# Kernel optimization log

Measured on AMD Instinct MI355X. Metric: run time of the kernel, lower is better.

Reference implementation:

```python
import jax, jax.numpy as jnp
import numpy as np
import math
from jax import lax

N = 5          # kernel_size (hard-coded PHT assumes 5x5)
K = N // 2     # 2
EPS = 1e-6
THETA = 0.7

def _pht_kernel_np():
    # H_i = cos(2*pi*2*r^2 + 0*theta) on the 5x5 grid, times calibrated spectral weights, plus eps
    coords = np.arange(N, dtype=np.float32) - K
    gv, gu = np.meshgrid(coords, coords, indexing='ij')  # torch.meshgrid default is 'ij'
    r2 = (gu ** 2 + gv ** 2) / (K * K + EPS)
    H = np.cos(2.0 * math.pi * 2.0 * r2).astype(np.float32)
    target = np.zeros((N, N), np.float32)
    target[K, K] = -4.0
    target[K - 1, K] = 1.0
    target[K + 1, K] = 1.0
    target[K, K - 1] = 1.0
    target[K, K + 1] = 1.0
    sw = np.where(target != 0, target / H, 0.0).astype(np.float32)
    return (H * sw + EPS).astype(np.float32)  # (5,5)

def _rotation_maps_np():
    # Replicates rotate_kernel exactly: float32 cos/sin, int() truncation, later (h,w) overwrite.
    angles = np.linspace(0, 2 * np.pi, 8, endpoint=False)
    SH = np.zeros((8, N, N), np.int32)
    SW = np.zeros((8, N, N), np.int32)
    M = np.zeros((8, N, N), np.float32)
    for ai, a in enumerate(angles):
        c = float(np.cos(np.float32(a)))
        s = float(np.sin(np.float32(a)))
        for h in range(N):
            for w in range(N):
                rh = int(h * c + w * (-s))
                rw = int(h * s + w * c)
                if 0 <= rh < N and 0 <= rw < N:
                    SH[ai, rh, rw] = h
                    SW[ai, rh, rw] = w
                    M[ai, rh, rw] = 1.0
    return SH, SW, M

_PHT = jnp.asarray(_pht_kernel_np())                     # (5,5)
_sh, _sw, _m = _rotation_maps_np()
_SH = jnp.asarray(_sh)
_SW = jnp.asarray(_sw)
_MASK = jnp.asarray(_m)

def setup_inputs() -> dict:
    key = jax.random.key(0)
    k1, k2 = jax.random.split(key)
    x = jax.random.normal(k1, (32, 64, 128, 128), dtype=jnp.float32)
    weight = jax.random.normal(k2, (64, 64, 5, 5), dtype=jnp.float32) * 0.05
    alpha = jnp.ones((1,), dtype=jnp.float32)
    return {"x": x, "weight": weight, "alpha": alpha}

def reference(x, weight, alpha):
    # Branch 1: PHT-modulated weight, averaged over 8 SO(2) rotations.
    # pht_kernel is (C_in,1,5,5) with identical values per channel -> broadcast (5,5).
    w_eff = weight * alpha[0] * _PHT[None, None]          # (Co,Ci,5,5)
    # rotated[o,i,a,rh,rw] = w_eff[o,i,SH[a,rh,rw],SW[a,rh,rw]] * MASK
    rotated = w_eff[:, :, _SH, _SW] * _MASK               # (Co,Ci,8,5,5)
    # conv is linear in weight: mean of 8 convs == conv with mean kernel
    mean_k = rotated.mean(axis=2)                         # (Co,Ci,5,5)
    out = lax.conv_general_dilated(
        x, mean_k, window_strides=(1, 1), padding=[(2, 2), (2, 2)],
        dimension_numbers=("NCHW", "OIHW", "NCHW"))
    # Branch 2: 1x1 kernel_diff; rotation of a 1x1 kernel is identity, mean of 8 == single conv.
    kd = weight.sum(axis=(2, 3))                          # (Co,Ci)
    out_diff = jnp.einsum("oi,bihw->bohw", kd, x)
    return out - THETA * out_diff
```

## Files before the change

### kernel.cpp

```cpp
#include <hip/hip_runtime.h>
#include <stdint.h>

typedef __attribute__((ext_vector_type(8))) __bf16 bf16x8;
typedef __attribute__((ext_vector_type(16))) float f32x16;
typedef __attribute__((ext_vector_type(4))) unsigned int u32x4;
typedef __attribute__((ext_vector_type(4))) float f32x4;
typedef __attribute__((ext_vector_type(2))) float f32x2;
typedef unsigned int u32;
typedef unsigned short u16;

#define THETA 0.7f

__host__ __device__ constexpr float pht_val(int q) {
  return (q == 12) ? (-4.0f + 1e-6f)
       : (q == 7 || q == 11 || q == 13 || q == 17) ? (1.0f + 1e-6f)
       : 1e-6f;
}

__device__ __forceinline__ u16 f2bf(float v) {
  u32 u = __builtin_bit_cast(u32, v);
  return (u16)((u + 0x7fffu + ((u >> 16) & 1u)) >> 16);
}

__global__ __launch_bounds__(256) void k_prep(const float* __restrict__ wgt,
                                              const float* __restrict__ alpha,
                                              u16* __restrict__ apack) {
  int t = blockIdx.x * 256 + threadIdx.x;
  int o = t >> 6, ci = t & 63;
  const float* wp = wgt + ((size_t)(o * 64 + ci)) * 25;
  float wv[25], sumw = 0.f;
#pragma unroll
  for (int p = 0; p < 25; ++p) { wv[p] = wp[p]; sumw += wv[p]; }
  float keff[25];
#pragma unroll
  for (int p = 0; p < 25; ++p) keff[p] = pht_val(p) * wv[p];
  constexpr int TP[33] = {0,1,2,3,4,6,7,9,12,13,  0,1,2,3,4,  0, 0, 0,
                          0,5,10,15,20,  0,5,6,10,11,12,15,17,20,21};
  constexpr int TQ[33] = {5,6,12,17,23,10,16,22,20,21,  0,5,10,15,20,  5, 0, 5,
                          0,6,7,8,9,  5,6,2,12,8,4,17,9,23,14};
#pragma unroll
  for (int e = 0; e < 33; ++e) keff[TP[e]] += pht_val(TQ[e]) * wv[TQ[e]];

  float al = alpha[0];
  int kc = ci >> 4, oh = o >> 5;
  int lane = ((ci >> 3) & 1) * 32 + (o & 31);
#pragma unroll
  for (int p = 0; p < 25; ++p) {
    float v = al * (keff[p] * 0.125f);
    if (p == 12) v -= THETA * sumw;
    size_t idx = ((((size_t)p * 4 + kc) * 2 + oh) * 64 + lane) * 8 + (ci & 7);
    apack[idx] = f2bf(v);
  }
}

#define GSTR 1168
#define RSTR 2336
#define BUFSZ 18688

#define MM(A, B, C) __builtin_amdgcn_mfma_f32_32x32x16_bf16((A), __builtin_bit_cast(bf16x8, (B)), (C), 0, 0, 0)

#define PK2(A_, B_) ({ u32 r_;                                              \
    asm("v_cvt_pk_bf16_f32 %0, %1, %2" : "=v"(r_) : "v"(A_), "v"(B_));      \
    r_; })

#define LDBR(S, DX, KC) do {                                                \
    const char* pb_ = tile + (((KC) & 1) * BUFSZ) + cb0 + (DX) * 16;        \
    br##S##0 = *(const u32x4*)(pb_ + 0 * RSTR);                             \
    br##S##1 = *(const u32x4*)(pb_ + 1 * RSTR);                             \
    br##S##2 = *(const u32x4*)(pb_ + 2 * RSTR);                             \
    br##S##3 = *(const u32x4*)(pb_ + 3 * RSTR);                             \
    br##S##4 = *(const u32x4*)(pb_ + 4 * RSTR);                             \
    br##S##5 = *(const u32x4*)(pb_ + 5 * RSTR);                             \
    br##S##6 = *(const u32x4*)(pb_ + 6 * RSTR);                             \
    br##S##7 = *(const u32x4*)(pb_ + 7 * RSTR);                             \
  } while (0)

#define LDAF(S, DX, KC) do {                                                \
    af##S##0 = apb[(size_t)((0 * 5 + (DX)) * 512 + (KC) * 128)];            \
    af##S##1 = apb[(size_t)((1 * 5 + (DX)) * 512 + (KC) * 128)];            \
    af##S##2 = apb[(size_t)((2 * 5 + (DX)) * 512 + (KC) * 128)];            \
    af##S##3 = apb[(size_t)((3 * 5 + (DX)) * 512 + (KC) * 128)];            \
    af##S##4 = apb[(size_t)((4 * 5 + (DX)) * 512 + (KC) * 128)];            \
  } while (0)

#define BURST(S) do {                                                       \
    bf16x8 A_;                                                              \
    A_ = __builtin_bit_cast(bf16x8, af##S##0);                              \
    a0 = MM(A_, br##S##0, a0); a1 = MM(A_, br##S##1, a1);                   \
    a2 = MM(A_, br##S##2, a2); a3 = MM(A_, br##S##3, a3);                   \
    A_ = __builtin_bit_cast(bf16x8, af##S##1);                              \
    a0 = MM(A_, br##S##1, a0); a1 = MM(A_, br##S##2, a1);                   \
    a2 = MM(A_, br##S##3, a2); a3 = MM(A_, br##S##4, a3);                   \
    A_ = __builtin_bit_cast(bf16x8, af##S##2);                              \
    a0 = MM(A_, br##S##2, a0); a1 = MM(A_, br##S##3, a1);                   \
    a2 = MM(A_, br##S##4, a2); a3 = MM(A_, br##S##5, a3);                   \
    A_ = __builtin_bit_cast(bf16x8, af##S##3);                              \
    a0 = MM(A_, br##S##3, a0); a1 = MM(A_, br##S##4, a1);                   \
    a2 = MM(A_, br##S##5, a2); a3 = MM(A_, br##S##6, a3);                   \
    A_ = __builtin_bit_cast(bf16x8, af##S##4);                              \
    a0 = MM(A_, br##S##4, a0); a1 = MM(A_, br##S##5, a1);                   \
    a2 = MM(A_, br##S##6, a2); a3 = MM(A_, br##S##7, a3);                   \
  } while (0)

#define SGB __builtin_amdgcn_sched_group_barrier
#define SCHED_FULL() do {                                                   \
    SGB(0x020, 5, 0);                                                       \
    SGB(0x100, 2, 0); SGB(0x008, 5, 0);                                     \
    SGB(0x100, 2, 0); SGB(0x008, 5, 0);                                     \
    SGB(0x100, 2, 0); SGB(0x008, 5, 0);                                     \
    SGB(0x100, 2, 0); SGB(0x008, 5, 0);                                     \
  } while (0)

#define ITER(CUR, NXT, DXN, KCN) do {                                       \
    LDBR(NXT, DXN, KCN); LDAF(NXT, DXN, KCN); BURST(CUR); SCHED_FULL();     \
  } while (0)

#define TBAR() do {                                                         \
    asm volatile("s_waitcnt lgkmcnt(0)" ::: "memory");                      \
    __builtin_amdgcn_sched_barrier(0);                                      \
    __builtin_amdgcn_s_barrier();                                           \
    __builtin_amdgcn_sched_barrier(0);                                      \
  } while (0)

#define SLOADP(P) do {                                                      \
    if (rowok) {                                                            \
      const float* pm_ = xrow + (size_t)(16 * (P) + 8 * gp) * 16384 + pxm;  \
      sm0 = *(const f32x4*)(pm_);              sm1 = *(const f32x4*)(pm_ + 16384);      \
      sm2 = *(const f32x4*)(pm_ + 2 * 16384);  sm3 = *(const f32x4*)(pm_ + 3 * 16384);  \
      sm4 = *(const f32x4*)(pm_ + 4 * 16384);  sm5 = *(const f32x4*)(pm_ + 5 * 16384);  \
      sm6 = *(const f32x4*)(pm_ + 6 * 16384);  sm7 = *(const f32x4*)(pm_ + 7 * 16384);  \
    } else {                                                                \
      sm0 = 0; sm1 = 0; sm2 = 0; sm3 = 0; sm4 = 0; sm5 = 0; sm6 = 0; sm7 = 0; \
    }                                                                       \
    if (hdut) {                                                             \
      if (hok) {                                                            \
        const float* ph_ = xn + (size_t)hsy * 128                           \
                           + (size_t)(16 * (P) + 8 * hgp) * 16384 + hpx;    \
        sh0 = *(const f32x2*)(ph_);              sh1 = *(const f32x2*)(ph_ + 16384);     \
        sh2 = *(const f32x2*)(ph_ + 2 * 16384);  sh3 = *(const f32x2*)(ph_ + 3 * 16384); \
        sh4 = *(const f32x2*)(ph_ + 4 * 16384);  sh5 = *(const f32x2*)(ph_ + 5 * 16384); \
        sh6 = *(const f32x2*)(ph_ + 6 * 16384);  sh7 = *(const f32x2*)(ph_ + 7 * 16384); \
      } else {                                                              \
        sh0 = 0; sh1 = 0; sh2 = 0; sh3 = 0; sh4 = 0; sh5 = 0; sh6 = 0; sh7 = 0; \
      }                                                                     \
    }                                                                       \
  } while (0)

#define SWRITEP(P) do {                                                     \
    char* wb_ = tile + (((P) & 1) * BUFSZ) + rr * RSTR + gp * GSTR;         \
    u32x4 w_;                                                               \
    w_[0] = PK2(sm0.x, sm1.x); w_[1] = PK2(sm2.x, sm3.x);                   \
    w_[2] = PK2(sm4.x, sm5.x); w_[3] = PK2(sm6.x, sm7.x);                   \
    *(u32x4*)(wb_ + (cbm + 0) * 16) = w_;                                   \
    w_[0] = PK2(sm0.y, sm1.y); w_[1] = PK2(sm2.y, sm3.y);                   \
    w_[2] = PK2(sm4.y, sm5.y); w_[3] = PK2(sm6.y, sm7.y);                   \
    *(u32x4*)(wb_ + (cbm + 1) * 16) = w_;                                   \
    w_[0] = PK2(sm0.z, sm1.z); w_[1] = PK2(sm2.z, sm3.z);                   \
    w_[2] = PK2(sm4.z, sm5.z); w_[3] = PK2(sm6.z, sm7.z);                   \
    *(u32x4*)(wb_ + (cbm + 2) * 16) = w_;                                   \
    w_[0] = PK2(sm0.w, sm1.w); w_[1] = PK2(sm2.w, sm3.w);                   \
    w_[2] = PK2(sm4.w, sm5.w); w_[3] = PK2(sm6.w, sm7.w);                   \
    *(u32x4*)(wb_ + (cbm + 3) * 16) = w_;                                   \
    if (hdut) {                                                             \
      char* hb_ = tile + (((P) & 1) * BUFSZ) + hrr * RSTR + hgp * GSTR;     \
      u32x4 u_;                                                             \
      u_[0] = PK2(sh0.x, sh1.x); u_[1] = PK2(sh2.x, sh3.x);                 \
      u_[2] = PK2(sh4.x, sh5.x); u_[3] = PK2(sh6.x, sh7.x);                 \
      *(u32x4*)(hb_ + (hc + 0) * 16) = u_;                                  \
      u_[0] = PK2(sh0.y, sh1.y); u_[1] = PK2(sh2.y, sh3.y);                 \
      u_[2] = PK2(sh4.y, sh5.y); u_[3] = PK2(sh6.y, sh7.y);                 \
      *(u32x4*)(hb_ + (hc + 1) * 16) = u_;                                  \
    }                                                                       \
  } while (0)

#define CPHASE(SP, CP) do {                                                 \
    SLOADP(SP);                                                             \
    LDBR(A, 0, CP); LDAF(A, 0, CP);                                         \
    ITER(A, B, 1, CP);                                                      \
    ITER(B, A, 2, CP);                                                      \
    SWRITEP(SP);                                                            \
    ITER(A, B, 3, CP);                                                      \
    ITER(B, A, 4, CP);                                                      \
    BURST(A);                                                               \
    TBAR();                                                                 \
  } while (0)

__global__ __launch_bounds__(256, 2) void k_conv(const float* __restrict__ x,
                                                 const u32x4* __restrict__ apv,
                                                 float* __restrict__ out) {
  __shared__ char tile[2 * BUFSZ];
  int bid = blockIdx.x;
  int lg = (bid & 7) * 256 + (bid >> 3);
  int ph = lg & 1, yt = (lg >> 1) & 31, n = lg >> 6;
  int y0 = yt * 4, px0 = ph * 64;
  int tid = threadIdx.x;
  int l = tid & 63;

  const float* xn = x + (size_t)n * (64 * 16384);
  int rr = tid >> 5, qq = (tid >> 1) & 15, gp = tid & 1;
  int sy = y0 + rr - 2;
  bool rowok = (unsigned)sy < 128u;
  const float* xrow = xn + (size_t)(rowok ? sy : 0) * 128;
  int pxm = px0 + 4 * qq;
  int cbm = 4 + 4 * qq;
  bool hdut = tid < 32;
  int hrr = tid >> 2, hside = (tid >> 1) & 1, hgp = tid & 1;
  int hpx = hside ? px0 + 64 : px0 - 2;
  int hc = hside ? 68 : 2;
  int hsy = y0 + hrr - 2;
  bool hok = ((unsigned)hpx < 127u) && ((unsigned)hsy < 128u);
  if (!hok) hsy = 0; if (hpx < 0) hpx = 0;

  int wv = tid >> 6;
  int oh = wv >> 1, q32 = wv & 1;
  int l31 = l & 31, lhi = l >> 5;
  const u32x4* apb = apv + (size_t)(oh * 64 + l);
  int cb0 = lhi * GSTR + (q32 * 32 + l31 + 2) * 16;

  f32x4 sm0, sm1, sm2, sm3, sm4, sm5, sm6, sm7;
  f32x2 sh0, sh1, sh2, sh3, sh4, sh5, sh6, sh7;
  u32x4 brA0, brA1, brA2, brA3, brA4, brA5, brA6, brA7;
  u32x4 brB0, brB1, brB2, brB3, brB4, brB5, brB6, brB7;
  u32x4 afA0, afA1, afA2, afA3, afA4;
  u32x4 afB0, afB1, afB2, afB3, afB4;
  f32x16 a0 = 0, a1 = 0, a2 = 0, a3 = 0;

  SLOADP(0);
  SWRITEP(0);
  TBAR();
  CPHASE(1, 0);
  CPHASE(2, 1);
  CPHASE(3, 2);
  LDBR(A, 0, 3); LDAF(A, 0, 3);
  ITER(A, B, 1, 3);
  ITER(B, A, 2, 3);
  ITER(A, B, 3, 3);
  ITER(B, A, 4, 3);
  BURST(A);

  float* ob = out + ((size_t)(n * 64 + oh * 32) * 128 + y0) * 128
              + px0 + q32 * 32 + l31;
#pragma unroll
  for (int rg = 0; rg < 16; ++rg) {
    int orow = (rg & 3) + 8 * (rg >> 2) + 4 * lhi;
    float* obr = ob + (size_t)orow * 16384;
    obr[0]   = a0[rg];
    obr[128] = a1[rg];
    obr[256] = a2[rg];
    obr[384] = a3[rg];
  }
}

extern "C" void kernel_launch(void* const* d_in, const int* in_sizes, int n_in,
                              void* d_out, int out_size, void* d_ws, size_t ws_size,
                              hipStream_t stream) {
  const float* x     = (const float*)d_in[0];
  const float* wgt   = (const float*)d_in[1];
  const float* alpha = (const float*)d_in[2];
  float* out = (float*)d_out;

  u16* apack = (u16*)d_ws;

  k_prep<<<16,   256, 0, stream>>>(wgt, alpha, apack);
  k_conv<<<2048, 256, 0, stream>>>(x, (const u32x4*)apack, out);
}
```

Before: 113.1 us.

## Double block threads, split output rows across waves, drop manual software pipelining

Raises k_conv to 512 threads per block (8 waves), each wave now computing 2 output rows with two accumulators instead of 4, and the staging loads split across twice as many threads. The explicit double-buffered register prefetch (A/B register sets) and sched_group_barrier scheduling are removed in favour of a simple load-then-MFMA sequence. The aim is lower register pressure and higher occupancy for better latency hiding. In exchange, each A-fragment is reused for fewer MFMAs, more global A loads are issued, and the hand-tuned instruction interleaving is lost.

```diff
diff --git a/kernel.cpp b/kernel.cpp
--- a/kernel.cpp
+++ b/kernel.cpp
@@ -4,6 +4,7 @@
 typedef __attribute__((ext_vector_type(8))) __bf16 bf16x8;
 typedef __attribute__((ext_vector_type(16))) float f32x16;
 typedef __attribute__((ext_vector_type(4))) unsigned int u32x4;
+typedef __attribute__((ext_vector_type(2))) unsigned int u32x2;
 typedef __attribute__((ext_vector_type(4))) float f32x4;
 typedef __attribute__((ext_vector_type(2))) float f32x2;
 typedef unsigned int u32;
@@ -63,57 +64,39 @@
     asm("v_cvt_pk_bf16_f32 %0, %1, %2" : "=v"(r_) : "v"(A_), "v"(B_));      \
     r_; })
 
-#define LDBR(S, DX, KC) do {                                                \
-    const char* pb_ = tile + (((KC) & 1) * BUFSZ) + cb0 + (DX) * 16;        \
-    br##S##0 = *(const u32x4*)(pb_ + 0 * RSTR);                             \
-    br##S##1 = *(const u32x4*)(pb_ + 1 * RSTR);                             \
-    br##S##2 = *(const u32x4*)(pb_ + 2 * RSTR);                             \
-    br##S##3 = *(const u32x4*)(pb_ + 3 * RSTR);                             \
-    br##S##4 = *(const u32x4*)(pb_ + 4 * RSTR);                             \
-    br##S##5 = *(const u32x4*)(pb_ + 5 * RSTR);                             \
-    br##S##6 = *(const u32x4*)(pb_ + 6 * RSTR);                             \
-    br##S##7 = *(const u32x4*)(pb_ + 7 * RSTR);                             \
-  } while (0)
-
-#define LDAF(S, DX, KC) do {                                                \
-    af##S##0 = apb[(size_t)((0 * 5 + (DX)) * 512 + (KC) * 128)];            \
-    af##S##1 = apb[(size_t)((1 * 5 + (DX)) * 512 + (KC) * 128)];            \
-    af##S##2 = apb[(size_t)((2 * 5 + (DX)) * 512 + (KC) * 128)];            \
-    af##S##3 = apb[(size_t)((3 * 5 + (DX)) * 512 + (KC) * 128)];            \
-    af##S##4 = apb[(size_t)((4 * 5 + (DX)) * 512 + (KC) * 128)];            \
-  } while (0)
-
-#define BURST(S) do {                                                       \
+#define LDBR(DX, KC) do {                                                   \
+    const char* pb_ = tile + (((KC) & 1) * BUFSZ) + rbase + (DX) * 16;      \
+    br0 = *(const u32x4*)(pb_ + 0 * RSTR);                                  \
+    br1 = *(const u32x4*)(pb_ + 1 * RSTR);                                  \
+    br2 = *(const u32x4*)(pb_ + 2 * RSTR);                                  \
+    br3 = *(const u32x4*)(pb_ + 3 * RSTR);                                  \
+    br4 = *(const u32x4*)(pb_ + 4 * RSTR);                                  \
+    br5 = *(const u32x4*)(pb_ + 5 * RSTR);                                  \
+  } while (0)
+
+#define LDAF(DX, KC) do {                                                   \
+    af0 = apb[(size_t)((0 * 5 + (DX)) * 512 + (KC) * 128)];                 \
+    af1 = apb[(size_t)((1 * 5 + (DX)) * 512 + (KC) * 128)];                 \
+    af2 = apb[(size_t)((2 * 5 + (DX)) * 512 + (KC) * 128)];                 \
+    af3 = apb[(size_t)((3 * 5 + (DX)) * 512 + (KC) * 128)];                 \
+    af4 = apb[(size_t)((4 * 5 + (DX)) * 512 + (KC) * 128)];                 \
+  } while (0)
+
+#define BURST() do {                                                        \
     bf16x8 A_;                                                              \
-    A_ = __builtin_bit_cast(bf16x8, af##S##0);                              \
-    a0 = MM(A_, br##S##0, a0); a1 = MM(A_, br##S##1, a1);                   \
-    a2 = MM(A_, br##S##2, a2); a3 = MM(A_, br##S##3, a3);                   \
-    A_ = __builtin_bit_cast(bf16x8, af##S##1);                              \
-    a0 = MM(A_, br##S##1, a0); a1 = MM(A_, br##S##2, a1);                   \
-    a2 = MM(A_, br##S##3, a2); a3 = MM(A_, br##S##4, a3);                   \
-    A_ = __builtin_bit_cast(bf16x8, af##S##2);                              \
-    a0 = MM(A_, br##S##2, a0); a1 = MM(A_, br##S##3, a1);                   \
-    a2 = MM(A_, br##S##4, a2); a3 = MM(A_, br##S##5, a3);                   \
-    A_ = __builtin_bit_cast(bf16x8, af##S##3);                              \
-    a0 = MM(A_, br##S##3, a0); a1 = MM(A_, br##S##4, a1);                   \
-    a2 = MM(A_, br##S##5, a2); a3 = MM(A_, br##S##6, a3);                   \
-    A_ = __builtin_bit_cast(bf16x8, af##S##4);                              \
-    a0 = MM(A_, br##S##4, a0); a1 = MM(A_, br##S##5, a1);                   \
-    a2 = MM(A_, br##S##6, a2); a3 = MM(A_, br##S##7, a3);                   \
-  } while (0)
-
-#define SGB __builtin_amdgcn_sched_group_barrier
-#define SCHED_FULL() do {                                                   \
-    SGB(0x020, 5, 0);                                                       \
-    SGB(0x100, 2, 0); SGB(0x008, 5, 0);                                     \
-    SGB(0x100, 2, 0); SGB(0x008, 5, 0);                                     \
-    SGB(0x100, 2, 0); SGB(0x008, 5, 0);                                     \
-    SGB(0x100, 2, 0); SGB(0x008, 5, 0);                                     \
-  } while (0)
-
-#define ITER(CUR, NXT, DXN, KCN) do {                                       \
-    LDBR(NXT, DXN, KCN); LDAF(NXT, DXN, KCN); BURST(CUR); SCHED_FULL();     \
-  } while (0)
+    A_ = __builtin_bit_cast(bf16x8, af0);                                   \
+    a0 = MM(A_, br0, a0); a1 = MM(A_, br1, a1);                             \
+    A_ = __builtin_bit_cast(bf16x8, af1);                                   \
+    a0 = MM(A_, br1, a0); a1 = MM(A_, br2, a1);                             \
+    A_ = __builtin_bit_cast(bf16x8, af2);                                   \
+    a0 = MM(A_, br2, a0); a1 = MM(A_, br3, a1);                             \
+    A_ = __builtin_bit_cast(bf16x8, af3);                                   \
+    a0 = MM(A_, br3, a0); a1 = MM(A_, br4, a1);                             \
+    A_ = __builtin_bit_cast(bf16x8, af4);                                   \
+    a0 = MM(A_, br4, a0); a1 = MM(A_, br5, a1);                             \
+  } while (0)
+
+#define DXITER(DX, KC) do { LDBR(DX, KC); LDAF(DX, KC); BURST(); } while (0)
 
 #define TBAR() do {                                                         \
     asm volatile("s_waitcnt lgkmcnt(0)" ::: "memory");                      \
@@ -124,68 +107,57 @@
 
 #define SLOADP(P) do {                                                      \
     if (rowok) {                                                            \
-      const float* pm_ = xrow + (size_t)(16 * (P) + 8 * gp) * 16384 + pxm;  \
-      sm0 = *(const f32x4*)(pm_);              sm1 = *(const f32x4*)(pm_ + 16384);      \
-      sm2 = *(const f32x4*)(pm_ + 2 * 16384);  sm3 = *(const f32x4*)(pm_ + 3 * 16384);  \
-      sm4 = *(const f32x4*)(pm_ + 4 * 16384);  sm5 = *(const f32x4*)(pm_ + 5 * 16384);  \
-      sm6 = *(const f32x4*)(pm_ + 6 * 16384);  sm7 = *(const f32x4*)(pm_ + 7 * 16384);  \
-    } else {                                                                \
-      sm0 = 0; sm1 = 0; sm2 = 0; sm3 = 0; sm4 = 0; sm5 = 0; sm6 = 0; sm7 = 0; \
-    }                                                                       \
+      const float* pm_ = xrow + (size_t)(16 * (P) + 8 * gp + 4 * hh) * 16384 + pxm; \
+      sm0 = *(const f32x4*)(pm_);                                           \
+      sm1 = *(const f32x4*)(pm_ + 16384);                                   \
+      sm2 = *(const f32x4*)(pm_ + 2 * 16384);                               \
+      sm3 = *(const f32x4*)(pm_ + 3 * 16384);                               \
+    } else { sm0 = 0; sm1 = 0; sm2 = 0; sm3 = 0; }                          \
     if (hdut) {                                                             \
       if (hok) {                                                            \
         const float* ph_ = xn + (size_t)hsy * 128                           \
-                           + (size_t)(16 * (P) + 8 * hgp) * 16384 + hpx;    \
-        sh0 = *(const f32x2*)(ph_);              sh1 = *(const f32x2*)(ph_ + 16384);     \
-        sh2 = *(const f32x2*)(ph_ + 2 * 16384);  sh3 = *(const f32x2*)(ph_ + 3 * 16384); \
-        sh4 = *(const f32x2*)(ph_ + 4 * 16384);  sh5 = *(const f32x2*)(ph_ + 5 * 16384); \
-        sh6 = *(const f32x2*)(ph_ + 6 * 16384);  sh7 = *(const f32x2*)(ph_ + 7 * 16384); \
-      } else {                                                              \
-        sh0 = 0; sh1 = 0; sh2 = 0; sh3 = 0; sh4 = 0; sh5 = 0; sh6 = 0; sh7 = 0; \
-      }                                                                     \
+                           + (size_t)(16 * (P) + 8 * hgp + 4 * hhh) * 16384 + hpx; \
+        sh0 = *(const f32x2*)(ph_);                                         \
+        sh1 = *(const f32x2*)(ph_ + 16384);                                 \
+        sh2 = *(const f32x2*)(ph_ + 2 * 16384);                             \
+        sh3 = *(const f32x2*)(ph_ + 3 * 16384);                             \
+      } else { sh0 = 0; sh1 = 0; sh2 = 0; sh3 = 0; }                        \
     }                                                                       \
   } while (0)
 
 #define SWRITEP(P) do {                                                     \
-    char* wb_ = tile + (((P) & 1) * BUFSZ) + rr * RSTR + gp * GSTR;         \
-    u32x4 w_;                                                               \
+    char* wb_ = tile + (((P) & 1) * BUFSZ) + rr * RSTR + gp * GSTR + hh * 8;\
+    u32x2 w_;                                                               \
     w_[0] = PK2(sm0.x, sm1.x); w_[1] = PK2(sm2.x, sm3.x);                   \
-    w_[2] = PK2(sm4.x, sm5.x); w_[3] = PK2(sm6.x, sm7.x);                   \
-    *(u32x4*)(wb_ + (cbm + 0) * 16) = w_;                                   \
+    *(u32x2*)(wb_ + (cbm + 0) * 16) = w_;                                   \
     w_[0] = PK2(sm0.y, sm1.y); w_[1] = PK2(sm2.y, sm3.y);                   \
-    w_[2] = PK2(sm4.y, sm5.y); w_[3] = PK2(sm6.y, sm7.y);                   \
-    *(u32x4*)(wb_ + (cbm + 1) * 16) = w_;                                   \
+    *(u32x2*)(wb_ + (cbm + 1) * 16) = w_;                                   \
     w_[0] = PK2(sm0.z, sm1.z); w_[1] = PK2(sm2.z, sm3.z);                   \
-    w_[2] = PK2(sm4.z, sm5.z); w_[3] = PK2(sm6.z, sm7.z);                   \
-    *(u32x4*)(wb_ + (cbm + 2) * 16) = w_;                                   \
+    *(u32x2*)(wb_ + (cbm + 2) * 16) = w_;                                   \
     w_[0] = PK2(sm0.w, sm1.w); w_[1] = PK2(sm2.w, sm3.w);                   \
-    w_[2] = PK2(sm4.w, sm5.w); w_[3] = PK2(sm6.w, sm7.w);                   \
-    *(u32x4*)(wb_ + (cbm + 3) * 16) = w_;                                   \
+    *(u32x2*)(wb_ + (cbm + 3) * 16) = w_;                                   \
     if (hdut) {                                                             \
-      char* hb_ = tile + (((P) & 1) * BUFSZ) + hrr * RSTR + hgp * GSTR;     \
-      u32x4 u_;                                                             \
+      char* hb_ = tile + (((P) & 1) * BUFSZ) + hrr * RSTR + hgp * GSTR + hhh * 8; \
+      u32x2 u_;                                                             \
       u_[0] = PK2(sh0.x, sh1.x); u_[1] = PK2(sh2.x, sh3.x);                 \
-      u_[2] = PK2(sh4.x, sh5.x); u_[3] = PK2(sh6.x, sh7.x);                 \
-      *(u32x4*)(hb_ + (hc + 0) * 16) = u_;                                  \
+      *(u32x2*)(hb_ + (hc + 0) * 16) = u_;                                  \
       u_[0] = PK2(sh0.y, sh1.y); u_[1] = PK2(sh2.y, sh3.y);                 \
-      u_[2] = PK2(sh4.y, sh5.y); u_[3] = PK2(sh6.y, sh7.y);                 \
-      *(u32x4*)(hb_ + (hc + 1) * 16) = u_;                                  \
+      *(u32x2*)(hb_ + (hc + 1) * 16) = u_;                                  \
     }                                                                       \
   } while (0)
 
 #define CPHASE(SP, CP) do {                                                 \
     SLOADP(SP);                                                             \
-    LDBR(A, 0, CP); LDAF(A, 0, CP);                                         \
-    ITER(A, B, 1, CP);                                                      \
-    ITER(B, A, 2, CP);                                                      \
+    DXITER(0, CP);                                                          \
+    DXITER(1, CP);                                                          \
+    DXITER(2, CP);                                                          \
+    DXITER(3, CP);                                                          \
     SWRITEP(SP);                                                            \
-    ITER(A, B, 3, CP);                                                      \
-    ITER(B, A, 4, CP);                                                      \
-    BURST(A);                                                               \
+    DXITER(4, CP);                                                          \
     TBAR();                                                                 \
   } while (0)
 
-__global__ __launch_bounds__(256, 2) void k_conv(const float* __restrict__ x,
+__global__ __launch_bounds__(512, 4) void k_conv(const float* __restrict__ x,
                                                  const u32x4* __restrict__ apv,
                                                  float* __restrict__ out) {
   __shared__ char tile[2 * BUFSZ];
@@ -197,14 +169,15 @@
   int l = tid & 63;
 
   const float* xn = x + (size_t)n * (64 * 16384);
-  int rr = tid >> 5, qq = (tid >> 1) & 15, gp = tid & 1;
+  int rr = tid >> 6;
+  int qq = (tid >> 2) & 15, gp = (tid >> 1) & 1, hh = tid & 1;
   int sy = y0 + rr - 2;
   bool rowok = (unsigned)sy < 128u;
   const float* xrow = xn + (size_t)(rowok ? sy : 0) * 128;
   int pxm = px0 + 4 * qq;
   int cbm = 4 + 4 * qq;
-  bool hdut = tid < 32;
-  int hrr = tid >> 2, hside = (tid >> 1) & 1, hgp = tid & 1;
+  bool hdut = tid < 64;
+  int hrr = tid >> 3, hside = (tid >> 2) & 1, hgp = (tid >> 1) & 1, hhh = tid & 1;
   int hpx = hside ? px0 + 64 : px0 - 2;
   int hc = hside ? 68 : 2;
   int hsy = y0 + hrr - 2;
@@ -212,18 +185,16 @@
   if (!hok) hsy = 0; if (hpx < 0) hpx = 0;
 
   int wv = tid >> 6;
-  int oh = wv >> 1, q32 = wv & 1;
+  int oh = wv >> 2, q32 = (wv >> 1) & 1, rp = wv & 1;
   int l31 = l & 31, lhi = l >> 5;
   const u32x4* apb = apv + (size_t)(oh * 64 + l);
-  int cb0 = lhi * GSTR + (q32 * 32 + l31 + 2) * 16;
-
-  f32x4 sm0, sm1, sm2, sm3, sm4, sm5, sm6, sm7;
-  f32x2 sh0, sh1, sh2, sh3, sh4, sh5, sh6, sh7;
-  u32x4 brA0, brA1, brA2, brA3, brA4, brA5, brA6, brA7;
-  u32x4 brB0, brB1, brB2, brB3, brB4, brB5, brB6, brB7;
-  u32x4 afA0, afA1, afA2, afA3, afA4;
-  u32x4 afB0, afB1, afB2, afB3, afB4;
-  f32x16 a0 = 0, a1 = 0, a2 = 0, a3 = 0;
+  int rbase = 2 * rp * RSTR + lhi * GSTR + (q32 * 32 + l31 + 2) * 16;
+
+  f32x4 sm0, sm1, sm2, sm3;
+  f32x2 sh0, sh1, sh2, sh3;
+  u32x4 br0, br1, br2, br3, br4, br5;
+  u32x4 af0, af1, af2, af3, af4;
+  f32x16 a0 = 0, a1 = 0;
 
   SLOADP(0);
   SWRITEP(0);
@@ -231,14 +202,13 @@
   CPHASE(1, 0);
   CPHASE(2, 1);
   CPHASE(3, 2);
-  LDBR(A, 0, 3); LDAF(A, 0, 3);
-  ITER(A, B, 1, 3);
-  ITER(B, A, 2, 3);
-  ITER(A, B, 3, 3);
-  ITER(B, A, 4, 3);
-  BURST(A);
-
-  float* ob = out + ((size_t)(n * 64 + oh * 32) * 128 + y0) * 128
+  DXITER(0, 3);
+  DXITER(1, 3);
+  DXITER(2, 3);
+  DXITER(3, 3);
+  DXITER(4, 3);
+
+  float* ob = out + ((size_t)(n * 64 + oh * 32) * 128 + (y0 + 2 * rp)) * 128
               + px0 + q32 * 32 + l31;
 #pragma unroll
   for (int rg = 0; rg < 16; ++rg) {
@@ -246,8 +216,6 @@
     float* obr = ob + (size_t)orow * 16384;
     obr[0]   = a0[rg];
     obr[128] = a1[rg];
-    obr[256] = a2[rg];
-    obr[384] = a3[rg];
   }
 }
 
@@ -262,5 +230,5 @@
   u16* apack = (u16*)d_ws;
 
   k_prep<<<16,   256, 0, stream>>>(wgt, alpha, apack);
-  k_conv<<<2048, 256, 0, stream>>>(x, (const u32x4*)apack, out);
-}
+  k_conv<<<2048, 512, 0, stream>>>(x, (const u32x4*)apack, out);
+}
```

Result: slower. 138.1 us (+22.1%).
